# Optimization experiments

Hardware: AMD Instinct MI355X
Metric: run time of the kernel (lower is better)

Reference implementation:

```python
import jax, jax.numpy as jnp
import numpy as np

B, T, IN, H, OUT = 256, 100, 128, 1024, 35
BITS = 4
SLOPE = 25.0
THR_H = 1.0
THR_O = 1.0
BETA1, BETA2, BETA3, BETA4 = 0.9, 0.85, 0.8, 0.95


def fake_quant(w, w_min, w_max, bits=BITS):
    # FakeQuantize in training mode: STE -> forward value is quantized, grad passes through clamp
    levels = 2 ** bits
    scale = (w_max - w_min) / (levels - 1)
    wc = jnp.clip(w, w_min, w_max)
    q = jnp.round((wc - w_min) / scale) * scale + w_min
    return wc + jax.lax.stop_gradient(q - wc)


@jax.custom_vjp
def spike(x):
    # Heaviside forward, fast-sigmoid surrogate backward (snn.surrogate.fast_sigmoid)
    return (x > 0).astype(x.dtype)

def _spike_fwd(x):
    return (x > 0).astype(x.dtype), x

def _spike_bwd(x, g):
    return (g / (SLOPE * jnp.abs(x) + 1.0) ** 2,)

spike.defvjp(_spike_fwd, _spike_bwd)


def lif_step(cur, mem, beta, thr, reset_mechanism):
    # snntorch Leaky (reset_delay semantics): reset computed from previous mem, detached
    reset = jax.lax.stop_gradient((mem > thr).astype(cur.dtype))
    base = beta * mem + cur
    if reset_mechanism == "subtract":
        mem_new = base - reset * thr
    else:  # "zero"
        mem_new = base - reset * base
    spk = spike(mem_new - thr)
    return spk, mem_new


def setup_inputs() -> dict:
    key = jax.random.key(0)
    ks = jax.random.split(key, 5)
    x = jax.random.normal(ks[0], (B, T, IN), dtype=jnp.float32)
    # QuantLinear init: uniform(w_min, w_max); fc1 uses (-0.5, 0.5), others (0.001, 1.0)
    w1 = jax.random.uniform(ks[1], (H, IN), minval=-0.5, maxval=0.5, dtype=jnp.float32)
    w2 = jax.random.uniform(ks[2], (H, H), minval=0.001, maxval=1.0, dtype=jnp.float32)
    w3 = jax.random.uniform(ks[3], (H, H), minval=0.001, maxval=1.0, dtype=jnp.float32)
    w4 = jax.random.uniform(ks[4], (OUT, H), minval=0.001, maxval=1.0, dtype=jnp.float32)
    return {"x": x, "w1": w1, "w2": w2, "w3": w3, "w4": w4}


def reference(x, w1, w2, w3, w4):
    # hoist weight quantization out of the time loop (identical math each step)
    q1 = fake_quant(w1, -0.5, 0.5)
    q2 = fake_quant(w2, 0.001, 1.0)
    q3 = fake_quant(w3, 0.001, 1.0)
    q4 = fake_quant(w4, 0.001, 1.0)
    xs = jnp.transpose(x, (1, 0, 2)) / 15.0  # [T, B, IN]
    Bx = x.shape[0]

    def step(carry, xt):
        m1, m2, m3, m4 = carry
        s1, m1 = lif_step(xt @ q1.T, m1, BETA1, THR_H, "subtract")
        s2, m2 = lif_step(s1 @ q2.T, m2, BETA2, THR_H, "subtract")
        s3, m3 = lif_step(s2 @ q3.T, m3, BETA3, THR_H, "subtract")
        s4, m4 = lif_step(s3 @ q4.T, m4, BETA4, THR_O, "zero")
        return (m1, m2, m3, m4), (s1, s2, s3, s4, m4)

    init = (jnp.zeros((Bx, H), x.dtype), jnp.zeros((Bx, H), x.dtype),
            jnp.zeros((Bx, H), x.dtype), jnp.zeros((Bx, OUT), x.dtype))
    _, (spk1, spk2, spk3, spk4, mem4) = jax.lax.scan(step, init, xs)
    # stacked along time dim 0, matching torch.stack(dim=0)
    return spk1, spk2, spk3, spk4, mem4
```

## Files before the change

kernel.cpp:

```cpp
#include <hip/hip_runtime.h>
#include <stdint.h>

#define NB  256
#define NT  100
#define NIN 128
#define NH  1024
#define NOUT 35

#define O_SPK2 26214400ull
#define O_SPK3 52428800ull
#define O_SPK4 78643200ull
#define O_MEM4 79539200ull

#define WS_XT   0ull
#define WS_Q1T  13107200ull
#define WS_K2T  13631488ull
#define WS_K3T  14680064ull
#define WS_K4T  15728640ull
#define WS_RS2  15777792ull
#define WS_RS3  15781888ull
#define WS_RS4  15785984ull

#define S2C ((float)((1.0 - 0.001) / 15.0))
#define S1C ((float)(1.0 / 15.0))

__global__ void k_prep(const float* __restrict__ x, const float* __restrict__ w1,
                       const float* __restrict__ w2, const float* __restrict__ w3,
                       const float* __restrict__ w4, uint8_t* __restrict__ ws)
{
  long long id = (long long)blockIdx.x * 256 + threadIdx.x;
  if (id < 1048576) {
    int i = (int)(id >> 10), j = (int)(id & 1023);
    float wv = w2[(size_t)j * 1024 + i];
    float wc = fminf(fmaxf(wv, 0.001f), 1.0f);
    ws[WS_K2T + id] = (uint8_t)(int)rintf((wc - 0.001f) / S2C);
    return;
  }
  id -= 1048576;
  if (id < 1048576) {
    int i = (int)(id >> 10), j = (int)(id & 1023);
    float wv = w3[(size_t)j * 1024 + i];
    float wc = fminf(fmaxf(wv, 0.001f), 1.0f);
    ws[WS_K3T + id] = (uint8_t)(int)rintf((wc - 0.001f) / S2C);
    return;
  }
  id -= 1048576;
  if (id < 49152) {
    int i = (int)(id / 48), j = (int)(id % 48);
    uint8_t v = 0;
    if (j < NOUT) {
      float wv = w4[(size_t)j * 1024 + i];
      float wc = fminf(fmaxf(wv, 0.001f), 1.0f);
      v = (uint8_t)(int)rintf((wc - 0.001f) / S2C);
    }
    ws[WS_K4T + id] = v;
    return;
  }
  id -= 49152;
  if (id < 131072) {
    int i = (int)(id >> 10), j = (int)(id & 1023);
    float wv = w1[(size_t)j * 128 + i];
    float wc = fminf(fmaxf(wv, -0.5f), 0.5f);
    float q = rintf((wc + 0.5f) / S1C) * S1C - 0.5f;
    ((float*)(ws + WS_Q1T))[id] = q;
    return;
  }
  id -= 131072;
  if (id < 3276800) {
    int row = (int)(id >> 7), i = (int)(id & 127);
    int tt = row >> 8, bb = row & 255;
    ((float*)(ws + WS_XT))[id] = x[((size_t)bb * NT + tt) * NIN + i] / 15.0f;
  }
}

__global__ void k_rowsum(const float* __restrict__ w2, const float* __restrict__ w3,
                         const float* __restrict__ w4, uint8_t* __restrict__ ws)
{
  int bid = blockIdx.x, tid = threadIdx.x;
  const float* W;
  uint32_t* o;
  if (bid < 1024)      { W = w2 + (size_t)bid * 1024;          o = (uint32_t*)(ws + WS_RS2) + bid; }
  else if (bid < 2048) { W = w3 + (size_t)(bid - 1024) * 1024; o = (uint32_t*)(ws + WS_RS3) + (bid - 1024); }
  else                 { W = w4 + (size_t)(bid - 2048) * 1024; o = (uint32_t*)(ws + WS_RS4) + (bid - 2048); }
  uint32_t s = 0;
  for (int i = tid; i < 1024; i += 256) {
    float wc = fminf(fmaxf(W[i], 0.001f), 1.0f);
    s += (uint32_t)(int)rintf((wc - 0.001f) / S2C);
  }
  #pragma unroll
  for (int off = 32; off; off >>= 1) s += (uint32_t)__shfl_down((int)s, off);
  __shared__ uint32_t red[4];
  if ((tid & 63) == 0) red[tid >> 6] = s;
  __syncthreads();
  if (tid == 0) *o = red[0] + red[1] + red[2] + red[3];
}

__global__ __launch_bounds__(256) void k_cur1(const uint8_t* __restrict__ ws, float* __restrict__ out)
{
  __shared__ float xsT[128 * 68];
  __shared__ float qch[16 * 256];
  const float* xt  = (const float*)(ws + WS_XT);
  const float* q1T = (const float*)(ws + WS_Q1T);
  const int tid = threadIdx.x;
  const int rb = blockIdx.x >> 2, cb = blockIdx.x & 3;
  const int jI = tid & 63, rI = tid >> 6;
  const int j4 = jI * 4, r16 = rI * 16;

  #pragma unroll
  for (int k = 0; k < 32; ++k) {
    int e = tid + k * 256;
    int r = e >> 7, i = e & 127;
    xsT[i * 68 + r] = xt[((size_t)rb * 64 + r) * 128 + i];
  }
  float acc[16][4];
  #pragma unroll
  for (int d = 0; d < 16; ++d) {
    acc[d][0] = 0.f; acc[d][1] = 0.f; acc[d][2] = 0.f; acc[d][3] = 0.f;
  }
  for (int ic = 0; ic < 8; ++ic) {
    __syncthreads();
    #pragma unroll
    for (int k = 0; k < 16; ++k) {
      int e = tid + k * 256;
      int ii = e >> 8, j = e & 255;
      qch[ii * 256 + j] = q1T[((size_t)(ic * 16 + ii) << 10) + cb * 256 + j];
    }
    __syncthreads();
    #pragma unroll
    for (int ii = 0; ii < 16; ++ii) {
      int i = ic * 16 + ii;
      const float4 q  = *(const float4*)&qch[ii * 256 + j4];
      const float4 xa = *(const float4*)&xsT[i * 68 + r16];
      const float4 xb = *(const float4*)&xsT[i * 68 + r16 + 4];
      const float4 xc = *(const float4*)&xsT[i * 68 + r16 + 8];
      const float4 xd = *(const float4*)&xsT[i * 68 + r16 + 12];
      float xr[16];
      xr[0]=xa.x; xr[1]=xa.y; xr[2]=xa.z; xr[3]=xa.w;
      xr[4]=xb.x; xr[5]=xb.y; xr[6]=xb.z; xr[7]=xb.w;
      xr[8]=xc.x; xr[9]=xc.y; xr[10]=xc.z; xr[11]=xc.w;
      xr[12]=xd.x; xr[13]=xd.y; xr[14]=xd.z; xr[15]=xd.w;
      #pragma unroll
      for (int d = 0; d < 16; ++d) {
        acc[d][0] = fmaf(xr[d], q.x, acc[d][0]);
        acc[d][1] = fmaf(xr[d], q.y, acc[d][1]);
        acc[d][2] = fmaf(xr[d], q.z, acc[d][2]);
        acc[d][3] = fmaf(xr[d], q.w, acc[d][3]);
      }
    }
  }
  #pragma unroll
  for (int d = 0; d < 16; ++d) {
    float4 v = make_float4(acc[d][0], acc[d][1], acc[d][2], acc[d][3]);
    *(float4*)&out[((size_t)rb * 64 + r16 + d) * 1024 + cb * 256 + j4] = v;
  }
}

__global__ __launch_bounds__(512) void k_main(const uint8_t* __restrict__ ws, float* out)
{
  const int b = blockIdx.x;
  const int tid = threadIdx.x;
  const int lane = tid & 63;
  const int wave = tid >> 6;
  const int g8 = wave;
  const int n64 = lane;

  const uint8_t* k2T = ws + WS_K2T;
  const uint8_t* k3T = ws + WS_K3T;
  const uint8_t* k4T = ws + WS_K4T;
  const uint32_t* rs2 = (const uint32_t*)(ws + WS_RS2);
  const uint32_t* rs3 = (const uint32_t*)(ws + WS_RS3);
  const uint32_t* rs4 = (const uint32_t*)(ws + WS_RS4);

  __shared__ uint16_t list[1024];
  __shared__ uint32_t pEa[2048];
  __shared__ uint32_t pOa[2048];
  __shared__ uint32_t wcnt[8];
  __shared__ uint32_t lpos;

  float m1[2] = {0.f, 0.f}, m2[2] = {0.f, 0.f}, m3[2] = {0.f, 0.f}, m4 = 0.f;
  uint32_t r2[2], r3[2], r4v = 0;
  r2[0] = rs2[tid]; r2[1] = rs2[tid + 512];
  r3[0] = rs3[tid]; r3[1] = rs3[tid + 512];
  if (tid < NOUT) r4v = rs4[tid];

  uint32_t nT, nL; bool cm;
  auto buildList = [&](bool sA, bool sB) {
    if (tid == 0) lpos = 0;
    uint64_t bA = __ballot(sA), bB = __ballot(sB);
    if (lane == 0) wcnt[wave] = (uint32_t)(__popcll(bA) + __popcll(bB));
    __syncthreads();
    nT = wcnt[0]+wcnt[1]+wcnt[2]+wcnt[3]+wcnt[4]+wcnt[5]+wcnt[6]+wcnt[7];
    cm = nT > 512;
    nL = cm ? (1024u - nT) : nT;
    uint64_t cA = cm ? ~bA : bA;
    uint64_t cB = cm ? ~bB : bB;
    uint32_t cnt = (uint32_t)(__popcll(cA) + __popcll(cB));
    uint32_t bs = 0;
    if (lane == 0) bs = atomicAdd(&lpos, cnt);
    bs = (uint32_t)__shfl((int)bs, 0);
    uint64_t ltm = (1ull << lane) - 1ull;
    if ((cA >> lane) & 1ull) list[bs + (uint32_t)__popcll(cA & ltm)] = (uint16_t)tid;
    if ((cB >> lane) & 1ull) list[bs + (uint32_t)__popcll(cA) + (uint32_t)__popcll(cB & ltm)] = (uint16_t)(tid + 512);
    __syncthreads();
  };

  auto gatherBig = [&](const uint8_t* mat) {
    uint32_t aE0=0,aE1=0,aE2=0,aE3=0,aO0=0,aO1=0,aO2=0,aO3=0;
    const uint8_t* bp = mat + (n64 << 4);
    for (uint32_t a = (uint32_t)g8; a < nL; a += 8) {
      uint32_t idx = list[a];
      const uint4 w = *(const uint4*)(bp + ((size_t)idx << 10));
      aE0 += w.x & 0x00FF00FFu; aO0 += (w.x >> 8) & 0x00FF00FFu;
      aE1 += w.y & 0x00FF00FFu; aO1 += (w.y >> 8) & 0x00FF00FFu;
      aE2 += w.z & 0x00FF00FFu; aO2 += (w.z >> 8) & 0x00FF00FFu;
      aE3 += w.w & 0x00FF00FFu; aO3 += (w.w >> 8) & 0x00FF00FFu;
    }
    int basei = (g8 << 8) + (n64 << 2);
    pEa[basei+0]=aE0; pEa[basei+1]=aE1; pEa[basei+2]=aE2; pEa[basei+3]=aE3;
    pOa[basei+0]=aO0; pOa[basei+1]=aO1; pOa[basei+2]=aO2; pOa[basei+3]=aO3;
  };

  auto gsum = [&](int j) -> uint32_t {
    int w = j >> 2;
    int sh = (j & 2) << 3;
    const uint32_t* P = (j & 1) ? pOa : pEa;
    uint32_t s = 0;
    #pragma unroll
    for (int gg = 0; gg < 8; ++gg) s += (P[(gg << 8) + w] >> sh) & 0xffffu;
    return s;
  };

  float curN[2];
  {
    size_t row0 = (size_t)b * NH;
    curN[0] = out[row0 + tid];
    curN[1] = out[row0 + tid + 512];
  }

  for (int t = 0; t < NT; ++t) {
    const size_t rowH = ((size_t)t * NB + b) * (size_t)NH;
    const size_t rowO = ((size_t)t * NB + b) * (size_t)NOUT;
    bool sA, sB;
    {
      float c0 = curN[0], c1 = curN[1];
      int tn = (t + 1 < NT) ? (t + 1) : t;
      size_t rowN = ((size_t)tn * NB + b) * (size_t)NH;
      curN[0] = out[rowN + tid];
      curN[1] = out[rowN + tid + 512];
      float rst0 = m1[0] > 1.0f ? 1.0f : 0.0f;
      m1[0] = fmaf(0.9f, m1[0], c0) - rst0;
      sA = (m1[0] - 1.0f) > 0.0f;
      out[rowH + tid] = sA ? 1.0f : 0.0f;
      float rst1 = m1[1] > 1.0f ? 1.0f : 0.0f;
      m1[1] = fmaf(0.9f, m1[1], c1) - rst1;
      sB = (m1[1] - 1.0f) > 0.0f;
      out[rowH + tid + 512] = sB ? 1.0f : 0.0f;
    }
    buildList(sA, sB);
    uint32_t n1 = nT, nl1 = nL; bool cm1 = cm;
    if (nl1) gatherBig(k2T);
    __syncthreads();
    {
      float nb = 0.001f * (float)n1;
      #pragma unroll
      for (int c = 0; c < 2; ++c) {
        int j = (c << 9) + tid;
        uint32_t gsv = nl1 ? gsum(j) : 0u;
        uint32_t K = cm1 ? (r2[c] - gsv) : gsv;
        float cur = fmaf(S2C, (float)K, nb);
        float rst = m2[c] > 1.0f ? 1.0f : 0.0f;
        m2[c] = fmaf(0.85f, m2[c], cur) - rst;
        bool sp = (m2[c] - 1.0f) > 0.0f;
        out[O_SPK2 + rowH + j] = sp ? 1.0f : 0.0f;
        if (c == 0) sA = sp; else sB = sp;
      }
    }
    buildList(sA, sB);
    uint32_t n2 = nT, nl2 = nL; bool cm2 = cm;
    if (nl2) gatherBig(k3T);
    __syncthreads();
    {
      float nb = 0.001f * (float)n2;
      #pragma unroll
      for (int c = 0; c < 2; ++c) {
        int j = (c << 9) + tid;
        uint32_t gsv = nl2 ? gsum(j) : 0u;
        uint32_t K = cm2 ? (r3[c] - gsv) : gsv;
        float cur = fmaf(S2C, (float)K, nb);
        float rst = m3[c] > 1.0f ? 1.0f : 0.0f;
        m3[c] = fmaf(0.8f, m3[c], cur) - rst;
        bool sp = (m3[c] - 1.0f) > 0.0f;
        out[O_SPK3 + rowH + j] = sp ? 1.0f : 0.0f;
        if (c == 0) sA = sp; else sB = sp;
      }
    }
    buildList(sA, sB);
    uint32_t n3 = nT, nl3 = nL; bool cm3 = cm;
    if (nl3 && n64 < 3) {
      uint32_t aE0=0,aE1=0,aE2=0,aE3=0,aO0=0,aO1=0,aO2=0,aO3=0;
      const uint8_t* bp = k4T + (n64 << 4);
      for (uint32_t a = (uint32_t)g8; a < nl3; a += 8) {
        uint32_t idx = list[a];
        const uint4 w = *(const uint4*)(bp + (size_t)idx * 48);
        aE0 += w.x & 0x00FF00FFu; aO0 += (w.x >> 8) & 0x00FF00FFu;
        aE1 += w.y & 0x00FF00FFu; aO1 += (w.y >> 8) & 0x00FF00FFu;
        aE2 += w.z & 0x00FF00FFu; aO2 += (w.z >> 8) & 0x00FF00FFu;
        aE3 += w.w & 0x00FF00FFu; aO3 += (w.w >> 8) & 0x00FF00FFu;
      }
      int basei = (g8 << 8) + (n64 << 2);
      pEa[basei+0]=aE0; pEa[basei+1]=aE1; pEa[basei+2]=aE2; pEa[basei+3]=aE3;
      pOa[basei+0]=aO0; pOa[basei+1]=aO1; pOa[basei+2]=aO2; pOa[basei+3]=aO3;
    }
    __syncthreads();
    if (tid < NOUT) {
      uint32_t gsv = nl3 ? gsum(tid) : 0u;
      uint32_t K = cm3 ? (r4v - gsv) : gsv;
      float cur = fmaf(S2C, (float)K, 0.001f * (float)n3);
      float rst = m4 > 1.0f ? 1.0f : 0.0f;
      float bsv = fmaf(0.95f, m4, cur);
      m4 = (rst > 0.0f) ? 0.0f : bsv;
      out[O_SPK4 + rowO + tid] = ((m4 - 1.0f) > 0.0f) ? 1.0f : 0.0f;
      out[O_MEM4 + rowO + tid] = m4;
    }
  }
}

extern "C" void kernel_launch(void* const* d_in, const int* in_sizes, int n_in,
                              void* d_out, int out_size, void* d_ws, size_t ws_size,
                              hipStream_t stream)
{
  const float* x  = (const float*)d_in[0];
  const float* w1 = (const float*)d_in[1];
  const float* w2 = (const float*)d_in[2];
  const float* w3 = (const float*)d_in[3];
  const float* w4 = (const float*)d_in[4];
  float* out = (float*)d_out;
  uint8_t* ws = (uint8_t*)d_ws;
  hipLaunchKernelGGL(k_prep,   dim3(21696), dim3(256), 0, stream, x, w1, w2, w3, w4, ws);
  hipLaunchKernelGGL(k_rowsum, dim3(2083),  dim3(256), 0, stream, w2, w3, w4, ws);
  hipLaunchKernelGGL(k_cur1,   dim3(1600),  dim3(256), 0, stream, ws, out);
  hipLaunchKernelGGL(k_main,   dim3(256),   dim3(512), 0, stream, ws, out);
}
```

Measured before the change: 684.7 us.

## Split recurrent loop into per-layer time scans plus int8 MFMA GEMMs

The single fused per-batch kernel that gathered sparse spike rows step by step is replaced by a layer-by-layer pipeline. Because each layer's input spikes do not depend on its own state, every layer first scans over time to produce a uint8 spike buffer, then one batched int8 MFMA GEMM over all 25600 (t,b) rows computes the next layer's integer currents. The x transpose and weight row-sum kernels are dropped and spike counts come from atomic ballot counts. This trades the latency-bound sequential loop for large bandwidth-heavy passes through extra workspace buffers.

```diff
diff --git a/kernel.cpp b/kernel.cpp
--- a/kernel.cpp
+++ b/kernel.cpp
@@ -6,57 +6,53 @@
 #define NIN 128
 #define NH  1024
 #define NOUT 35
+#define NR  25600
 
 #define O_SPK2 26214400ull
 #define O_SPK3 52428800ull
 #define O_SPK4 78643200ull
 #define O_MEM4 79539200ull
 
-#define WS_XT   0ull
-#define WS_Q1T  13107200ull
-#define WS_K2T  13631488ull
-#define WS_K3T  14680064ull
-#define WS_K4T  15728640ull
-#define WS_RS2  15777792ull
-#define WS_RS3  15781888ull
-#define WS_RS4  15785984ull
+#define WS_KBUF 0ull
+#define WS_SPKB 52428800ull
+#define WS_K2B  78643200ull
+#define WS_K3B  79691776ull
+#define WS_K4B  80740352ull
+#define WS_Q1T  80871424ull
+#define WS_N1   81395712ull
+#define WS_N2   81498112ull
+#define WS_N3   81600512ull
 
 #define S2C ((float)((1.0 - 0.001) / 15.0))
 #define S1C ((float)(1.0 / 15.0))
 
-__global__ void k_prep(const float* __restrict__ x, const float* __restrict__ w1,
-                       const float* __restrict__ w2, const float* __restrict__ w3,
-                       const float* __restrict__ w4, uint8_t* __restrict__ ws)
+typedef int v4i __attribute__((ext_vector_type(4)));
+
+__device__ __forceinline__ void async16(const void* g, void* l) {
+  __builtin_amdgcn_global_load_lds((const __attribute__((address_space(1))) uint32_t*)g,
+                                   (__attribute__((address_space(3))) uint32_t*)l, 16, 0, 0);
+}
+
+__device__ __forceinline__ uint8_t qk(float w) {
+  float wc = fminf(fmaxf(w, 0.001f), 1.0f);
+  return (uint8_t)(int)rintf((wc - 0.001f) / S2C);
+}
+
+__global__ void k_prep(const float* __restrict__ w1, const float* __restrict__ w2,
+                       const float* __restrict__ w3, const float* __restrict__ w4,
+                       uint8_t* __restrict__ ws)
 {
   long long id = (long long)blockIdx.x * 256 + threadIdx.x;
-  if (id < 1048576) {
-    int i = (int)(id >> 10), j = (int)(id & 1023);
-    float wv = w2[(size_t)j * 1024 + i];
-    float wc = fminf(fmaxf(wv, 0.001f), 1.0f);
-    ws[WS_K2T + id] = (uint8_t)(int)rintf((wc - 0.001f) / S2C);
+  if (id < 1048576) { ws[WS_K2B + id] = qk(w2[id]); return; }
+  id -= 1048576;
+  if (id < 1048576) { ws[WS_K3B + id] = qk(w3[id]); return; }
+  id -= 1048576;
+  if (id < 131072) {
+    int j = (int)(id >> 10), i = (int)(id & 1023);
+    ws[WS_K4B + id] = (j < NOUT) ? qk(w4[(size_t)j * 1024 + i]) : (uint8_t)0;
     return;
   }
-  id -= 1048576;
-  if (id < 1048576) {
-    int i = (int)(id >> 10), j = (int)(id & 1023);
-    float wv = w3[(size_t)j * 1024 + i];
-    float wc = fminf(fmaxf(wv, 0.001f), 1.0f);
-    ws[WS_K3T + id] = (uint8_t)(int)rintf((wc - 0.001f) / S2C);
-    return;
-  }
-  id -= 1048576;
-  if (id < 49152) {
-    int i = (int)(id / 48), j = (int)(id % 48);
-    uint8_t v = 0;
-    if (j < NOUT) {
-      float wv = w4[(size_t)j * 1024 + i];
-      float wc = fminf(fmaxf(wv, 0.001f), 1.0f);
-      v = (uint8_t)(int)rintf((wc - 0.001f) / S2C);
-    }
-    ws[WS_K4T + id] = v;
-    return;
-  }
-  id -= 49152;
+  id -= 131072;
   if (id < 131072) {
     int i = (int)(id >> 10), j = (int)(id & 1023);
     float wv = w1[(size_t)j * 128 + i];
@@ -66,43 +62,19 @@
     return;
   }
   id -= 131072;
-  if (id < 3276800) {
-    int row = (int)(id >> 7), i = (int)(id & 127);
-    int tt = row >> 8, bb = row & 255;
-    ((float*)(ws + WS_XT))[id] = x[((size_t)bb * NT + tt) * NIN + i] / 15.0f;
-  }
-}
-
-__global__ void k_rowsum(const float* __restrict__ w2, const float* __restrict__ w3,
-                         const float* __restrict__ w4, uint8_t* __restrict__ ws)
-{
-  int bid = blockIdx.x, tid = threadIdx.x;
-  const float* W;
-  uint32_t* o;
-  if (bid < 1024)      { W = w2 + (size_t)bid * 1024;          o = (uint32_t*)(ws + WS_RS2) + bid; }
-  else if (bid < 2048) { W = w3 + (size_t)(bid - 1024) * 1024; o = (uint32_t*)(ws + WS_RS3) + (bid - 1024); }
-  else                 { W = w4 + (size_t)(bid - 2048) * 1024; o = (uint32_t*)(ws + WS_RS4) + (bid - 2048); }
-  uint32_t s = 0;
-  for (int i = tid; i < 1024; i += 256) {
-    float wc = fminf(fmaxf(W[i], 0.001f), 1.0f);
-    s += (uint32_t)(int)rintf((wc - 0.001f) / S2C);
-  }
-  #pragma unroll
-  for (int off = 32; off; off >>= 1) s += (uint32_t)__shfl_down((int)s, off);
-  __shared__ uint32_t red[4];
-  if ((tid & 63) == 0) red[tid >> 6] = s;
-  __syncthreads();
-  if (tid == 0) *o = red[0] + red[1] + red[2] + red[3];
-}
-
-__global__ __launch_bounds__(256) void k_cur1(const uint8_t* __restrict__ ws, float* __restrict__ out)
+  if (id < 76800) ((uint32_t*)(ws + WS_N1))[id] = 0;
+}
+
+__global__ __launch_bounds__(256) void k_cur1(const float* __restrict__ x,
+                                              const uint8_t* __restrict__ ws,
+                                              float* __restrict__ out)
 {
   __shared__ float xsT[128 * 68];
   __shared__ float qch[16 * 256];
-  const float* xt  = (const float*)(ws + WS_XT);
   const float* q1T = (const float*)(ws + WS_Q1T);
   const int tid = threadIdx.x;
   const int rb = blockIdx.x >> 2, cb = blockIdx.x & 3;
+  const int t = rb >> 2, b0 = (rb & 3) * 64;
   const int jI = tid & 63, rI = tid >> 6;
   const int j4 = jI * 4, r16 = rI * 16;
 
@@ -110,13 +82,11 @@
   for (int k = 0; k < 32; ++k) {
     int e = tid + k * 256;
     int r = e >> 7, i = e & 127;
-    xsT[i * 68 + r] = xt[((size_t)rb * 64 + r) * 128 + i];
+    xsT[i * 68 + r] = x[((size_t)(b0 + r) * NT + t) * NIN + i] / 15.0f;
   }
   float acc[16][4];
   #pragma unroll
-  for (int d = 0; d < 16; ++d) {
-    acc[d][0] = 0.f; acc[d][1] = 0.f; acc[d][2] = 0.f; acc[d][3] = 0.f;
-  }
+  for (int d = 0; d < 16; ++d) { acc[d][0]=0.f; acc[d][1]=0.f; acc[d][2]=0.f; acc[d][3]=0.f; }
   for (int ic = 0; ic < 8; ++ic) {
     __syncthreads();
     #pragma unroll
@@ -155,173 +125,145 @@
   }
 }
 
-__global__ __launch_bounds__(512) void k_main(const uint8_t* __restrict__ ws, float* out)
+__global__ __launch_bounds__(256) void k_scan1(uint8_t* __restrict__ ws, float* __restrict__ out)
+{
+  const int tid = threadIdx.x;
+  const int b = blockIdx.x >> 2;
+  const int j = (blockIdx.x & 3) * 256 + tid;
+  uint8_t* spkb = ws + WS_SPKB;
+  uint32_t* n1 = (uint32_t*)(ws + WS_N1);
+  const size_t stride = (size_t)NB * NH;
+  size_t idx = (size_t)b * NH + j;
+  float m = 0.f;
+  float c = out[idx];
+  for (int t = 0; t < NT; ++t) {
+    float cn = (t + 1 < NT) ? out[idx + stride] : 0.f;
+    float rst = m > 1.0f ? 1.0f : 0.0f;
+    m = fmaf(0.9f, m, c) - rst;
+    bool sp = (m - 1.0f) > 0.0f;
+    out[idx] = sp ? 1.0f : 0.0f;
+    spkb[idx] = sp ? 1 : 0;
+    unsigned long long bal = __ballot(sp);
+    if ((tid & 63) == 0) atomicAdd((unsigned int*)&n1[t * NB + b], (unsigned)__popcll(bal));
+    idx += stride; c = cn;
+  }
+}
+
+__global__ __launch_bounds__(256) void k_gemm(const uint8_t* __restrict__ A,
+                                              const uint8_t* __restrict__ Bm,
+                                              uint16_t* __restrict__ C, int ncb)
+{
+  __shared__ uint8_t sA[16384];
+  __shared__ uint8_t sB[16384];
+  const int tid = threadIdx.x, lane = tid & 63, wave = tid >> 6;
+  const int lm = lane & 15, lk = lane >> 4;
+  const int rb = blockIdx.x, jb = blockIdx.y;
+  const int mw = wave & 1, nw = wave >> 1;
+  v4i acc[4][4];
+  #pragma unroll
+  for (int a = 0; a < 4; ++a)
+    #pragma unroll
+    for (int bb = 0; bb < 4; ++bb) { acc[a][bb][0]=0; acc[a][bb][1]=0; acc[a][bb][2]=0; acc[a][bb][3]=0; }
+
+  for (int kk = 0; kk < 1024; kk += 128) {
+    __syncthreads();
+    #pragma unroll
+    for (int q = 0; q < 8; ++q) {
+      int cid = wave * 8 + q;
+      if (cid < 16) {
+        int kh = cid >> 3, cm = cid & 7;
+        const uint8_t* g = A + (size_t)(rb * 128 + cm * 16 + lm) * 1024 + kk + kh * 64 + (lk << 4);
+        async16(g, sA + cid * 1024);
+      } else {
+        int cb2 = cid - 16;
+        int kh = cb2 >> 3, cn = cb2 & 7;
+        const uint8_t* g = Bm + (size_t)(jb * 128 + cn * 16 + lm) * 1024 + kk + kh * 64 + (lk << 4);
+        async16(g, sB + cb2 * 1024);
+      }
+    }
+    __syncthreads();
+    #pragma unroll
+    for (int kh = 0; kh < 2; ++kh) {
+      v4i av[4], bv[4];
+      #pragma unroll
+      for (int mi = 0; mi < 4; ++mi)
+        av[mi] = *(const v4i*)(sA + (size_t)(kh * 8 + mw * 4 + mi) * 1024 + lane * 16);
+      #pragma unroll
+      for (int ni = 0; ni < 4; ++ni)
+        bv[ni] = *(const v4i*)(sB + (size_t)(kh * 8 + nw * 4 + ni) * 1024 + lane * 16);
+      #pragma unroll
+      for (int mi = 0; mi < 4; ++mi)
+        #pragma unroll
+        for (int ni = 0; ni < 4; ++ni)
+          acc[mi][ni] = __builtin_amdgcn_mfma_i32_16x16x64_i8(av[mi], bv[ni], acc[mi][ni], 0, 0, 0);
+    }
+  }
+  const int rowb = rb * 128 + mw * 64;
+  const int colb = jb * 128 + nw * 64;
+  const int strideC = ncb * 128;
+  #pragma unroll
+  for (int mi = 0; mi < 4; ++mi)
+    #pragma unroll
+    for (int ni = 0; ni < 4; ++ni)
+      #pragma unroll
+      for (int r = 0; r < 4; ++r) {
+        int row = rowb + mi * 16 + (lane >> 4) * 4 + r;
+        int col = colb + ni * 16 + (lane & 15);
+        C[(size_t)row * strideC + col] = (uint16_t)acc[mi][ni][r];
+      }
+}
+
+__global__ __launch_bounds__(256) void k_scan23(const uint16_t* __restrict__ Kin,
+                                                const uint32_t* __restrict__ nprev,
+                                                uint32_t* __restrict__ nout,
+                                                float beta,
+                                                float* __restrict__ outB,
+                                                uint8_t* __restrict__ spkb)
+{
+  const int tid = threadIdx.x;
+  const int b = blockIdx.x >> 2;
+  const int j = (blockIdx.x & 3) * 256 + tid;
+  const size_t stride = (size_t)NB * NH;
+  size_t idx = (size_t)b * NH + j;
+  float m = 0.f;
+  uint16_t kv = Kin[idx];
+  for (int t = 0; t < NT; ++t) {
+    uint16_t kn = (t + 1 < NT) ? Kin[idx + stride] : (uint16_t)0;
+    float nb = 0.001f * (float)nprev[t * NB + b];
+    float cur = fmaf(S2C, (float)kv, nb);
+    float rst = m > 1.0f ? 1.0f : 0.0f;
+    m = fmaf(beta, m, cur) - rst;
+    bool sp = (m - 1.0f) > 0.0f;
+    outB[idx] = sp ? 1.0f : 0.0f;
+    spkb[idx] = sp ? 1 : 0;
+    unsigned long long bal = __ballot(sp);
+    if ((tid & 63) == 0) atomicAdd((unsigned int*)&nout[t * NB + b], (unsigned)__popcll(bal));
+    idx += stride; kv = kn;
+  }
+}
+
+__global__ __launch_bounds__(64) void k_scan4(const uint8_t* __restrict__ ws, float* __restrict__ out)
 {
   const int b = blockIdx.x;
-  const int tid = threadIdx.x;
-  const int lane = tid & 63;
-  const int wave = tid >> 6;
-  const int g8 = wave;
-  const int n64 = lane;
-
-  const uint8_t* k2T = ws + WS_K2T;
-  const uint8_t* k3T = ws + WS_K3T;
-  const uint8_t* k4T = ws + WS_K4T;
-  const uint32_t* rs2 = (const uint32_t*)(ws + WS_RS2);
-  const uint32_t* rs3 = (const uint32_t*)(ws + WS_RS3);
-  const uint32_t* rs4 = (const uint32_t*)(ws + WS_RS4);
-
-  __shared__ uint16_t list[1024];
-  __shared__ uint32_t pEa[2048];
-  __shared__ uint32_t pOa[2048];
-  __shared__ uint32_t wcnt[8];
-  __shared__ uint32_t lpos;
-
-  float m1[2] = {0.f, 0.f}, m2[2] = {0.f, 0.f}, m3[2] = {0.f, 0.f}, m4 = 0.f;
-  uint32_t r2[2], r3[2], r4v = 0;
-  r2[0] = rs2[tid]; r2[1] = rs2[tid + 512];
-  r3[0] = rs3[tid]; r3[1] = rs3[tid + 512];
-  if (tid < NOUT) r4v = rs4[tid];
-
-  uint32_t nT, nL; bool cm;
-  auto buildList = [&](bool sA, bool sB) {
-    if (tid == 0) lpos = 0;
-    uint64_t bA = __ballot(sA), bB = __ballot(sB);
-    if (lane == 0) wcnt[wave] = (uint32_t)(__popcll(bA) + __popcll(bB));
-    __syncthreads();
-    nT = wcnt[0]+wcnt[1]+wcnt[2]+wcnt[3]+wcnt[4]+wcnt[5]+wcnt[6]+wcnt[7];
-    cm = nT > 512;
-    nL = cm ? (1024u - nT) : nT;
-    uint64_t cA = cm ? ~bA : bA;
-    uint64_t cB = cm ? ~bB : bB;
-    uint32_t cnt = (uint32_t)(__popcll(cA) + __popcll(cB));
-    uint32_t bs = 0;
-    if (lane == 0) bs = atomicAdd(&lpos, cnt);
-    bs = (uint32_t)__shfl((int)bs, 0);
-    uint64_t ltm = (1ull << lane) - 1ull;
-    if ((cA >> lane) & 1ull) list[bs + (uint32_t)__popcll(cA & ltm)] = (uint16_t)tid;
-    if ((cB >> lane) & 1ull) list[bs + (uint32_t)__popcll(cA) + (uint32_t)__popcll(cB & ltm)] = (uint16_t)(tid + 512);
-    __syncthreads();
-  };
-
-  auto gatherBig = [&](const uint8_t* mat) {
-    uint32_t aE0=0,aE1=0,aE2=0,aE3=0,aO0=0,aO1=0,aO2=0,aO3=0;
-    const uint8_t* bp = mat + (n64 << 4);
-    for (uint32_t a = (uint32_t)g8; a < nL; a += 8) {
-      uint32_t idx = list[a];
-      const uint4 w = *(const uint4*)(bp + ((size_t)idx << 10));
-      aE0 += w.x & 0x00FF00FFu; aO0 += (w.x >> 8) & 0x00FF00FFu;
-      aE1 += w.y & 0x00FF00FFu; aO1 += (w.y >> 8) & 0x00FF00FFu;
-      aE2 += w.z & 0x00FF00FFu; aO2 += (w.z >> 8) & 0x00FF00FFu;
-      aE3 += w.w & 0x00FF00FFu; aO3 += (w.w >> 8) & 0x00FF00FFu;
-    }
-    int basei = (g8 << 8) + (n64 << 2);
-    pEa[basei+0]=aE0; pEa[basei+1]=aE1; pEa[basei+2]=aE2; pEa[basei+3]=aE3;
-    pOa[basei+0]=aO0; pOa[basei+1]=aO1; pOa[basei+2]=aO2; pOa[basei+3]=aO3;
-  };
-
-  auto gsum = [&](int j) -> uint32_t {
-    int w = j >> 2;
-    int sh = (j & 2) << 3;
-    const uint32_t* P = (j & 1) ? pOa : pEa;
-    uint32_t s = 0;
-    #pragma unroll
-    for (int gg = 0; gg < 8; ++gg) s += (P[(gg << 8) + w] >> sh) & 0xffffu;
-    return s;
-  };
-
-  float curN[2];
-  {
-    size_t row0 = (size_t)b * NH;
-    curN[0] = out[row0 + tid];
-    curN[1] = out[row0 + tid + 512];
-  }
-
+  const int j = threadIdx.x;
+  const uint16_t* K4 = (const uint16_t*)(ws + WS_KBUF);
+  const uint32_t* n3 = (const uint32_t*)(ws + WS_N3);
+  size_t idx = (size_t)b * 128 + j;
+  const size_t stride = (size_t)NB * 128;
+  float m = 0.f;
+  uint16_t kv = (j < NOUT) ? K4[idx] : (uint16_t)0;
   for (int t = 0; t < NT; ++t) {
-    const size_t rowH = ((size_t)t * NB + b) * (size_t)NH;
-    const size_t rowO = ((size_t)t * NB + b) * (size_t)NOUT;
-    bool sA, sB;
-    {
-      float c0 = curN[0], c1 = curN[1];
-      int tn = (t + 1 < NT) ? (t + 1) : t;
-      size_t rowN = ((size_t)tn * NB + b) * (size_t)NH;
-      curN[0] = out[rowN + tid];
-      curN[1] = out[rowN + tid + 512];
-      float rst0 = m1[0] > 1.0f ? 1.0f : 0.0f;
-      m1[0] = fmaf(0.9f, m1[0], c0) - rst0;
-      sA = (m1[0] - 1.0f) > 0.0f;
-      out[rowH + tid] = sA ? 1.0f : 0.0f;
-      float rst1 = m1[1] > 1.0f ? 1.0f : 0.0f;
-      m1[1] = fmaf(0.9f, m1[1], c1) - rst1;
-      sB = (m1[1] - 1.0f) > 0.0f;
-      out[rowH + tid + 512] = sB ? 1.0f : 0.0f;
-    }
-    buildList(sA, sB);
-    uint32_t n1 = nT, nl1 = nL; bool cm1 = cm;
-    if (nl1) gatherBig(k2T);
-    __syncthreads();
-    {
-      float nb = 0.001f * (float)n1;
-      #pragma unroll
-      for (int c = 0; c < 2; ++c) {
-        int j = (c << 9) + tid;
-        uint32_t gsv = nl1 ? gsum(j) : 0u;
-        uint32_t K = cm1 ? (r2[c] - gsv) : gsv;
-        float cur = fmaf(S2C, (float)K, nb);
-        float rst = m2[c] > 1.0f ? 1.0f : 0.0f;
-        m2[c] = fmaf(0.85f, m2[c], cur) - rst;
-        bool sp = (m2[c] - 1.0f) > 0.0f;
-        out[O_SPK2 + rowH + j] = sp ? 1.0f : 0.0f;
-        if (c == 0) sA = sp; else sB = sp;
-      }
-    }
-    buildList(sA, sB);
-    uint32_t n2 = nT, nl2 = nL; bool cm2 = cm;
-    if (nl2) gatherBig(k3T);
-    __syncthreads();
-    {
-      float nb = 0.001f * (float)n2;
-      #pragma unroll
-      for (int c = 0; c < 2; ++c) {
-        int j = (c << 9) + tid;
-        uint32_t gsv = nl2 ? gsum(j) : 0u;
-        uint32_t K = cm2 ? (r3[c] - gsv) : gsv;
-        float cur = fmaf(S2C, (float)K, nb);
-        float rst = m3[c] > 1.0f ? 1.0f : 0.0f;
-        m3[c] = fmaf(0.8f, m3[c], cur) - rst;
-        bool sp = (m3[c] - 1.0f) > 0.0f;
-        out[O_SPK3 + rowH + j] = sp ? 1.0f : 0.0f;
-        if (c == 0) sA = sp; else sB = sp;
-      }
-    }
-    buildList(sA, sB);
-    uint32_t n3 = nT, nl3 = nL; bool cm3 = cm;
-    if (nl3 && n64 < 3) {
-      uint32_t aE0=0,aE1=0,aE2=0,aE3=0,aO0=0,aO1=0,aO2=0,aO3=0;
-      const uint8_t* bp = k4T + (n64 << 4);
-      for (uint32_t a = (uint32_t)g8; a < nl3; a += 8) {
-        uint32_t idx = list[a];
-        const uint4 w = *(const uint4*)(bp + (size_t)idx * 48);
-        aE0 += w.x & 0x00FF00FFu; aO0 += (w.x >> 8) & 0x00FF00FFu;
-        aE1 += w.y & 0x00FF00FFu; aO1 += (w.y >> 8) & 0x00FF00FFu;
-        aE2 += w.z & 0x00FF00FFu; aO2 += (w.z >> 8) & 0x00FF00FFu;
-        aE3 += w.w & 0x00FF00FFu; aO3 += (w.w >> 8) & 0x00FF00FFu;
-      }
-      int basei = (g8 << 8) + (n64 << 2);
-      pEa[basei+0]=aE0; pEa[basei+1]=aE1; pEa[basei+2]=aE2; pEa[basei+3]=aE3;
-      pOa[basei+0]=aO0; pOa[basei+1]=aO1; pOa[basei+2]=aO2; pOa[basei+3]=aO3;
-    }
-    __syncthreads();
-    if (tid < NOUT) {
-      uint32_t gsv = nl3 ? gsum(tid) : 0u;
-      uint32_t K = cm3 ? (r4v - gsv) : gsv;
-      float cur = fmaf(S2C, (float)K, 0.001f * (float)n3);
-      float rst = m4 > 1.0f ? 1.0f : 0.0f;
-      float bsv = fmaf(0.95f, m4, cur);
-      m4 = (rst > 0.0f) ? 0.0f : bsv;
-      out[O_SPK4 + rowO + tid] = ((m4 - 1.0f) > 0.0f) ? 1.0f : 0.0f;
-      out[O_MEM4 + rowO + tid] = m4;
-    }
+    uint16_t kn = (t + 1 < NT && j < NOUT) ? K4[idx + stride] : (uint16_t)0;
+    float cur = fmaf(S2C, (float)kv, 0.001f * (float)n3[t * NB + b]);
+    float rst = m > 1.0f ? 1.0f : 0.0f;
+    float bsv = fmaf(0.95f, m, cur);
+    m = (rst > 0.0f) ? 0.0f : bsv;
+    if (j < NOUT) {
+      size_t rowO = ((size_t)t * NB + b) * NOUT + j;
+      out[O_SPK4 + rowO] = ((m - 1.0f) > 0.0f) ? 1.0f : 0.0f;
+      out[O_MEM4 + rowO] = m;
+    }
+    idx += stride; kv = kn;
   }
 }
 
@@ -336,8 +278,20 @@
   const float* w4 = (const float*)d_in[4];
   float* out = (float*)d_out;
   uint8_t* ws = (uint8_t*)d_ws;
-  hipLaunchKernelGGL(k_prep,   dim3(21696), dim3(256), 0, stream, x, w1, w2, w3, w4, ws);
-  hipLaunchKernelGGL(k_rowsum, dim3(2083),  dim3(256), 0, stream, w2, w3, w4, ws);
-  hipLaunchKernelGGL(k_cur1,   dim3(1600),  dim3(256), 0, stream, ws, out);
-  hipLaunchKernelGGL(k_main,   dim3(256),   dim3(512), 0, stream, ws, out);
-}
+
+  uint16_t* KBUF = (uint16_t*)(ws + WS_KBUF);
+  uint8_t*  SPKB = ws + WS_SPKB;
+  uint32_t* N1 = (uint32_t*)(ws + WS_N1);
+  uint32_t* N2 = (uint32_t*)(ws + WS_N2);
+  uint32_t* N3 = (uint32_t*)(ws + WS_N3);
+
+  hipLaunchKernelGGL(k_prep, dim3(9517), dim3(256), 0, stream, w1, w2, w3, w4, ws);
+  hipLaunchKernelGGL(k_cur1, dim3(1600), dim3(256), 0, stream, x, ws, out);
+  hipLaunchKernelGGL(k_scan1, dim3(1024), dim3(256), 0, stream, ws, out);
+  hipLaunchKernelGGL(k_gemm, dim3(200, 8), dim3(256), 0, stream, SPKB, ws + WS_K2B, KBUF, 8);
+  hipLaunchKernelGGL(k_scan23, dim3(1024), dim3(256), 0, stream, KBUF, N1, N2, 0.85f, out + O_SPK2, SPKB);
+  hipLaunchKernelGGL(k_gemm, dim3(200, 8), dim3(256), 0, stream, SPKB, ws + WS_K3B, KBUF, 8);
+  hipLaunchKernelGGL(k_scan23, dim3(1024), dim3(256), 0, stream, KBUF, N2, N3, 0.8f, out + O_SPK3, SPKB);
+  hipLaunchKernelGGL(k_gemm, dim3(200, 1), dim3(256), 0, stream, SPKB, ws + WS_K4B, KBUF, 1);
+  hipLaunchKernelGGL(k_scan4, dim3(256), dim3(64), 0, stream, ws, out);
+}
```

After: 747.2 us. 1.09x slower.
